# Kernel optimization log

Hardware: AMD Instinct MI355X
Metric: run time of the kernel (lower is better)

Reference implementation:

```python
import jax, jax.numpy as jnp
import numpy as np

B, N, D, E, HEADS = 2, 256, 768, 8192, 8
HD = D // HEADS
EPS = 1e-5


def _lin(x, w, b):
    return x @ w.T + b


def setup_inputs() -> dict:
    key = jax.random.key(0)
    ks = iter(jax.random.split(key, 64))

    def W(*s):
        return jax.random.normal(next(ks), s, jnp.float32) * 0.02

    inp = {
        "node_embeddings": jax.random.normal(next(ks), (B, N, D), jnp.float32),
        "edge_weights": jax.random.uniform(next(ks), (E,), jnp.float32),
        "edge_indices": jax.random.randint(next(ks), (E, 2), 0, N, jnp.int32),
        # object classifier: D->D->D//2->8
        "oc_w1": W(D, D), "oc_b1": jnp.zeros((D,), jnp.float32),
        "oc_w2": W(D // 2, D), "oc_b2": jnp.zeros((D // 2,), jnp.float32),
        "oc_w3": W(8, D // 2), "oc_b3": jnp.zeros((8,), jnp.float32),
        # importance predictor: D->D//2->D//4->1
        "ip_w1": W(D // 2, D), "ip_b1": jnp.zeros((D // 2,), jnp.float32),
        "ip_w2": W(D // 4, D // 2), "ip_b2": jnp.zeros((D // 4,), jnp.float32),
        "ip_w3": W(1, D // 4), "ip_b3": jnp.zeros((1,), jnp.float32),
        # relation classifier: 2D->D->D//2->8
        "rc_w1": W(D, 2 * D), "rc_b1": jnp.zeros((D,), jnp.float32),
        "rc_w2": W(D // 2, D), "rc_b2": jnp.zeros((D // 2,), jnp.float32),
        "rc_w3": W(8, D // 2), "rc_b3": jnp.zeros((8,), jnp.float32),
        # attention in/out projections
        "attn_in_w": W(3 * D, D), "attn_in_b": jnp.zeros((3 * D,), jnp.float32),
        "attn_out_w": W(D, D), "attn_out_b": jnp.zeros((D,), jnp.float32),
    }
    for l in range(3):
        inp[f"gnn{l}_ws"] = W(D, D)
        inp[f"gnn{l}_bs"] = jnp.zeros((D,), jnp.float32)
        inp[f"gnn{l}_wn"] = W(D, D)
        inp[f"gnn{l}_bn"] = jnp.zeros((D,), jnp.float32)
        inp[f"gnn{l}_g"] = jnp.ones((D,), jnp.float32)
        inp[f"gnn{l}_beta"] = jnp.zeros((D,), jnp.float32)
    return inp


def reference(node_embeddings, edge_weights, edge_indices,
              oc_w1, oc_b1, oc_w2, oc_b2, oc_w3, oc_b3,
              ip_w1, ip_b1, ip_w2, ip_b2, ip_w3, ip_b3,
              rc_w1, rc_b1, rc_w2, rc_b2, rc_w3, rc_b3,
              attn_in_w, attn_in_b, attn_out_w, attn_out_b,
              gnn0_ws, gnn0_bs, gnn0_wn, gnn0_bn, gnn0_g, gnn0_beta,
              gnn1_ws, gnn1_bs, gnn1_wn, gnn1_bn, gnn1_g, gnn1_beta,
              gnn2_ws, gnn2_bs, gnn2_wn, gnn2_bn, gnn2_g, gnn2_beta):
    x = node_embeddings  # [B,N,D]
    src, tgt = edge_indices[:, 0], edge_indices[:, 1]

    # object classifier (dropout is identity in eval)
    h = jax.nn.relu(_lin(x, oc_w1, oc_b1))
    h = jax.nn.relu(_lin(h, oc_w2, oc_b2))
    object_cls = jax.nn.softmax(_lin(h, oc_w3, oc_b3), axis=-1)

    # importance predictor
    h = jax.nn.relu(_lin(x, ip_w1, ip_b1))
    h = jax.nn.relu(_lin(h, ip_w2, ip_b2))
    importance = jax.nn.sigmoid(_lin(h, ip_w3, ip_b3))

    # 3 GNN layers: self-linear + weighted scatter-add neighbor aggregation
    g = x
    layers = [(gnn0_ws, gnn0_bs, gnn0_wn, gnn0_bn, gnn0_g, gnn0_beta),
              (gnn1_ws, gnn1_bs, gnn1_wn, gnn1_bn, gnn1_g, gnn1_beta),
              (gnn2_ws, gnn2_bs, gnn2_wn, gnn2_bn, gnn2_g, gnn2_beta)]
    for ws, bs, wn, bn, gm, bt in layers:
        self_f = _lin(g, ws, bs)
        # vectorized scatter-add: agg[b,tgt] += w_e * g[b,src]
        agg = jnp.zeros_like(g).at[:, tgt, :].add(edge_weights[None, :, None] * g[:, src, :])
        neigh_f = _lin(agg, wn, bn)
        o = jax.nn.relu(self_f + neigh_f)
        mu = o.mean(axis=-1, keepdims=True)
        var = o.var(axis=-1, keepdims=True)  # biased, as torch LayerNorm
        g = gm * (o - mu) / jnp.sqrt(var + EPS) + bt

    # multi-head self-attention (torch MultiheadAttention, batch_first)
    qkv = _lin(g, attn_in_w, attn_in_b)  # [B,N,3D]
    q, k, v = jnp.split(qkv, 3, axis=-1)

    def heads(t):
        return t.reshape(B, N, HEADS, HD).transpose(0, 2, 1, 3)  # [B,H,N,hd]

    q, k, v = heads(q), heads(k), heads(v)
    scores = jnp.einsum('bhqd,bhkd->bhqk', q, k) / jnp.sqrt(jnp.float32(HD))
    attn = jax.nn.softmax(scores, axis=-1)
    ctx = jnp.einsum('bhqk,bhkd->bhqd', attn, v).transpose(0, 2, 1, 3).reshape(B, N, D)
    attended = _lin(ctx, attn_out_w, attn_out_b)  # [B,N,D]
    attn_weights = attn.mean(axis=1)  # torch averages heads -> [B,N,N]

    # all O(N^2) upper-triangular pairs, same (i<j) row-major order as the loop
    ii, jj = np.triu_indices(N, k=1)
    pair = jnp.concatenate([attended[:, ii, :], attended[:, jj, :]], axis=-1)  # [B,P,2D]
    h = jax.nn.relu(_lin(pair, rc_w1, rc_b1))
    h = jax.nn.relu(_lin(h, rc_w2, rc_b2))
    relation = jax.nn.softmax(_lin(h, rc_w3, rc_b3), axis=-1)  # [B,P,8]

    return (object_cls, relation, importance, attended, attn_weights)
```

## Files before the change

kernel.cpp:

```cpp
#include <hip/hip_runtime.h>
#include <hip/hip_bf16.h>

typedef __bf16 bf16;
typedef __bf16 bf16x4 __attribute__((ext_vector_type(4)));
typedef __bf16 bf16x8 __attribute__((ext_vector_type(8)));
typedef float  f32x4  __attribute__((ext_vector_type(4)));

#define NB 2
#define NN 256
#define DD 768
#define EE 8192
#define NPAIR 32640

__device__ inline float wred_sum(float v) {
#pragma unroll
  for (int o = 32; o > 0; o >>= 1) v += __shfl_down(v, o, 64);
  return v;
}
__device__ inline float wred_max(float v) {
#pragma unroll
  for (int o = 32; o > 0; o >>= 1) v = fmaxf(v, __shfl_down(v, o, 64));
  return v;
}

typedef const __attribute__((address_space(1))) void GASV;
typedef __attribute__((address_space(3))) void LASV;
__device__ __forceinline__ void async_cp16(const void* g, void* l) {
  __builtin_amdgcn_global_load_lds((GASV*)g, (LASV*)l, 16, 0, 0);
}

struct CJob { const float* s; bf16* d; int n; };
struct CJobs { CJob j[15]; };
__global__ __launch_bounds__(256) void convert_jobs(CJobs jobs) {
  const CJob jb = jobs.j[blockIdx.y];
  int nv = jb.n >> 2;
  for (int i = blockIdx.x * 256 + threadIdx.x; i < nv; i += gridDim.x * 256) {
    float4 v = ((const float4*)jb.s)[i];
    bf16x4 pk = { (bf16)v.x, (bf16)v.y, (bf16)v.z, (bf16)v.w };
    *(bf16x4*)(jb.d + 4 * i) = pk;
  }
}

__device__ __forceinline__ void lin_body(
    const bf16* __restrict__ X, const bf16* __restrict__ W, int ldw, int wofs,
    const float* __restrict__ bias, const float* __restrict__ addF,
    bf16* __restrict__ outB, float* __restrict__ outF,
    int N, int K, int act)
{
  int tid = threadIdx.x;
  int wave = tid >> 6, lane = tid & 63, lr = lane & 15, lq = lane >> 4;
  int m0 = (blockIdx.x * 2 + wave) * 16;
  int n0 = blockIdx.y * 32;
  const bf16* xrow = X + (size_t)(m0 + lr) * K;
  const bf16* wbase = W + (size_t)wofs;
  f32x4 acc[2] = {};
  for (int k = 0; k < K; k += 32) {
    bf16x8 a = *(const bf16x8*)(xrow + k + lq * 8);
    bf16x8 b0 = *(const bf16x8*)(wbase + (size_t)(n0 + lr) * ldw + k + lq * 8);
    bf16x8 b1 = *(const bf16x8*)(wbase + (size_t)(n0 + 16 + lr) * ldw + k + lq * 8);
    acc[0] = __builtin_amdgcn_mfma_f32_16x16x32_bf16(a, b0, acc[0], 0, 0, 0);
    acc[1] = __builtin_amdgcn_mfma_f32_16x16x32_bf16(a, b1, acc[1], 0, 0, 0);
  }
#pragma unroll
  for (int t = 0; t < 2; ++t) {
    int col = n0 + t * 16 + lr;
    float bv = bias ? bias[col] : 0.0f;
#pragma unroll
    for (int r = 0; r < 4; ++r) {
      int row = m0 + lq * 4 + r;
      size_t o = (size_t)row * N + col;
      float v = acc[t][r] + bv;
      if (addF) v += addF[o];
      if (act) v = fmaxf(v, 0.0f);
      if (outB) outB[o] = (bf16)v;
      if (outF) outF[o] = v;
    }
  }
}

__global__ __launch_bounds__(128) void linear_mfma(
    const bf16* __restrict__ X, const bf16* __restrict__ W, int ldw, int wofs,
    const float* __restrict__ bias, const float* __restrict__ addF,
    bf16* __restrict__ outB, float* __restrict__ outF,
    int N, int K, int act)
{
  lin_body(X, W, ldw, wofs, bias, addF, outB, outF, N, K, act);
}

struct LinJob {
  const bf16* X; const bf16* W; int ldw; int wofs;
  const float* bias; const float* addF; bf16* outB; float* outF;
  int N, K, act, gy;
};
__global__ __launch_bounds__(128) void linear_mfma2(LinJob j0, LinJob j1)
{
  LinJob j = blockIdx.z ? j1 : j0;
  if ((int)blockIdx.y >= j.gy) return;
  lin_body(j.X, j.W, j.ldw, j.wofs, j.bias, j.addF, j.outB, j.outF, j.N, j.K, j.act);
}

__global__ __launch_bounds__(256) void build_buckets(
    const int* __restrict__ eidx, int* __restrict__ estart, int* __restrict__ bucket)
{
  __shared__ int tg[EE];
  __shared__ int cnt[256];
  __shared__ int sst[257];
  int t = threadIdx.x;
  cnt[t] = 0;
  for (int e = t; e < EE; e += 256) tg[e] = eidx[2 * e + 1];
  __syncthreads();
  for (int e = t; e < EE; e += 256) atomicAdd(&cnt[tg[e]], 1);
  __syncthreads();
  if (t == 0) { int s = 0; for (int i = 0; i < 256; ++i) { sst[i] = s; s += cnt[i]; } sst[256] = s; }
  __syncthreads();
  estart[t] = sst[t];
  if (t == 0) estart[256] = sst[256];
  cnt[t] = sst[t];
  __syncthreads();
  for (int e = t; e < EE; e += 256) {
    int p = atomicAdd(&cnt[tg[e]], 1);
    bucket[p] = e;
  }
}

__global__ __launch_bounds__(256) void gnn_agg(
    const bf16* __restrict__ g, const float* __restrict__ ew, const int* __restrict__ eidx,
    const int* __restrict__ estart, const int* __restrict__ bucket, bf16* __restrict__ agg)
{
  __shared__ int   ssrc[256];
  __shared__ float sw[256];
  int tgt = blockIdx.x, b = blockIdx.y, t = threadIdx.x;
  int s = estart[tgt], e = estart[tgt + 1];
  s = max(0, min(s, EE));
  e = max(s, min(e, EE));
  const bf16* gb = g + (size_t)b * NN * DD;
  float a0 = 0, a1 = 0, a2 = 0, a3 = 0;
  for (int base = s; base < e; base += 256) {
    int nchunk = min(256, e - base);
    if (t < nchunk) {
      int eid = bucket[base + t];
      eid = max(0, min(eid, EE - 1));
      ssrc[t] = eidx[2 * eid] & (NN - 1);
      sw[t] = ew[eid];
    }
    __syncthreads();
    if (t < 192) {
      for (int q = 0; q < nchunk; ++q) {
        float w = sw[q];
        bf16x4 v = *(const bf16x4*)(gb + (size_t)ssrc[q] * DD + 4 * t);
        a0 += w * (float)v[0]; a1 += w * (float)v[1];
        a2 += w * (float)v[2]; a3 += w * (float)v[3];
      }
    }
    __syncthreads();
  }
  if (t < 192) {
    bf16x4 o = { (bf16)a0, (bf16)a1, (bf16)a2, (bf16)a3 };
    *(bf16x4*)(agg + ((size_t)b * NN + tgt) * DD + 4 * t) = o;
  }
}

__global__ __launch_bounds__(256) void layer_norm(
    const float* __restrict__ o, const float* __restrict__ gm,
    const float* __restrict__ bt, bf16* __restrict__ gout)
{
  __shared__ float red[8];
  int row = blockIdx.x, t = threadIdx.x;
  const float* orow = o + (size_t)row * DD;
  float v0 = orow[t], v1 = orow[t + 256], v2 = orow[t + 512];
  float s = v0 + v1 + v2;
  float q = v0 * v0 + v1 * v1 + v2 * v2;
  float ws_ = wred_sum(s), wq = wred_sum(q);
  if ((t & 63) == 0) { red[t >> 6] = ws_; red[4 + (t >> 6)] = wq; }
  __syncthreads();
  float S = red[0] + red[1] + red[2] + red[3];
  float Q = red[4] + red[5] + red[6] + red[7];
  float mu = S * (1.0f / 768.0f);
  float var = Q * (1.0f / 768.0f) - mu * mu;
  float rstd = rsqrtf(var + 1e-5f);
  bf16* gr = gout + (size_t)row * DD;
  gr[t]       = (bf16)(gm[t]       * (v0 - mu) * rstd + bt[t]);
  gr[t + 256] = (bf16)(gm[t + 256] * (v1 - mu) * rstd + bt[t + 256]);
  gr[t + 512] = (bf16)(gm[t + 512] * (v2 - mu) * rstd + bt[t + 512]);
}

__global__ __launch_bounds__(256) void attn_kernel(
    const bf16* __restrict__ qkv, float* __restrict__ aw, bf16* __restrict__ ctx)
{
  __shared__ float qs[96];
  __shared__ float ps[256];
  __shared__ float part[192];
  __shared__ float red[8];
  int qi = blockIdx.x, h = blockIdx.y, b = blockIdx.z, t = threadIdx.x;
  const bf16* qrow = qkv + ((size_t)(b * NN + qi)) * 2304 + h * 96;
  if (t < 96) qs[t] = (float)qrow[t];
  __syncthreads();
  const bf16* krow = qkv + ((size_t)(b * NN + t)) * 2304 + 768 + h * 96;
  float s = 0;
#pragma unroll
  for (int i = 0; i < 12; ++i) {
    bf16x8 kv = *(const bf16x8*)(krow + 8 * i);
#pragma unroll
    for (int j = 0; j < 8; ++j) s += qs[8 * i + j] * (float)kv[j];
  }
  s *= 0.10206207261596577f;
  float wm = wred_max(s);
  if ((t & 63) == 0) red[t >> 6] = wm;
  __syncthreads();
  float MX = fmaxf(fmaxf(red[0], red[1]), fmaxf(red[2], red[3]));
  float e = expf(s - MX);
  float wsum = wred_sum(e);
  if ((t & 63) == 0) red[4 + (t >> 6)] = wsum;
  __syncthreads();
  float SUM = red[4] + red[5] + red[6] + red[7];
  float p = e / SUM;
  ps[t] = p;
  atomicAdd(&aw[((size_t)(b * NN + qi)) * NN + t], p * 0.125f);
  __syncthreads();
  if (t < 192) {
    int d = t % 96, half = t / 96;
    const bf16* vbase = qkv + (size_t)b * NN * 2304 + 1536 + h * 96 + d;
    float a0 = 0, a1 = 0, a2 = 0, a3 = 0;
    int k0 = half * 128;
    for (int k = k0; k < k0 + 128; k += 4) {
      a0 += ps[k]     * (float)vbase[(size_t)k * 2304];
      a1 += ps[k + 1] * (float)vbase[(size_t)(k + 1) * 2304];
      a2 += ps[k + 2] * (float)vbase[(size_t)(k + 2) * 2304];
      a3 += ps[k + 3] * (float)vbase[(size_t)(k + 3) * 2304];
    }
    part[t] = (a0 + a1) + (a2 + a3);
  }
  __syncthreads();
  if (t < 96)
    ctx[((size_t)(b * NN + qi)) * DD + h * 96 + t] = (bf16)(part[t] + part[t + 96]);
}

__global__ __launch_bounds__(256) void fc8_softmax(
    const bf16* __restrict__ h, const float* __restrict__ w,
    const float* __restrict__ bias, float* __restrict__ out)
{
  __shared__ float sw3[8 * 384];
  int t = threadIdx.x;
  for (int i = t; i < 8 * 384; i += 256) sw3[i] = w[i];
  __syncthreads();
  int wave = t >> 6, lane = t & 63;
  int k0 = lane * 6;
#pragma unroll
  for (int i = 0; i < 4; ++i) {
    int r = blockIdx.x * 16 + wave * 4 + i;
    const bf16* hr = h + (size_t)r * 384;
    float hv[6];
#pragma unroll
    for (int j = 0; j < 6; ++j) hv[j] = (float)hr[k0 + j];
    float lg[8];
#pragma unroll
    for (int c = 0; c < 8; ++c) {
      float p = 0;
#pragma unroll
      for (int j = 0; j < 6; ++j) p += hv[j] * sw3[c * 384 + k0 + j];
      lg[c] = wred_sum(p);
    }
    if (lane == 0) {
      float mx = lg[0] + bias[0];
#pragma unroll
      for (int c = 0; c < 8; ++c) { lg[c] += bias[c]; mx = fmaxf(mx, lg[c]); }
      float ex[8], sum = 0;
#pragma unroll
      for (int c = 0; c < 8; ++c) { ex[c] = expf(lg[c] - mx); sum += ex[c]; }
      float inv = 1.0f / sum;
#pragma unroll
      for (int c = 0; c < 8; ++c) out[(size_t)r * 8 + c] = ex[c] * inv;
    }
  }
}

__global__ __launch_bounds__(256) void fc1_sigmoid(
    const bf16* __restrict__ h, const float* __restrict__ w,
    const float* __restrict__ bias, float* __restrict__ out)
{
  __shared__ float sw1[192];
  int t = threadIdx.x;
  if (t < 192) sw1[t] = w[t];
  __syncthreads();
  int wave = t >> 6, lane = t & 63;
  int k0 = lane * 3;
#pragma unroll
  for (int i = 0; i < 4; ++i) {
    int r = blockIdx.x * 16 + wave * 4 + i;
    const bf16* hr = h + (size_t)r * 192;
    float p = (float)hr[k0] * sw1[k0] + (float)hr[k0 + 1] * sw1[k0 + 1]
            + (float)hr[k0 + 2] * sw1[k0 + 2];
    float s = wred_sum(p);
    if (lane == 0) out[r] = 1.0f / (1.0f + expf(-(s + bias[0])));
  }
}

__global__ void make_pairs(int2* __restrict__ pairs)
{
  int i = blockIdx.x;
  int off = i * 255 - (i * (i - 1)) / 2;
  for (int j = i + 1 + threadIdx.x; j < NN; j += blockDim.x)
    pairs[off + (j - i - 1)] = make_int2(i, j);
}

__global__ __launch_bounds__(256) void h2_gemm(
    const bf16* __restrict__ Af, const bf16* __restrict__ Bf,
    const bf16* __restrict__ w2, const float* __restrict__ b2,
    const int2* __restrict__ pairs, bf16* __restrict__ h2)
{
  __shared__ bf16 sh1[4][128][8];
  __shared__ bf16 sw2[4][192][8];
  __shared__ int rA[128], rB[128];
  int tid = threadIdx.x;
  int r0 = blockIdx.x * 128;
  int bb = (r0 >= NPAIR) ? 1 : 0;
  int n0 = blockIdx.y * 192;
  if (tid < 128) {
    int2 ij = pairs[r0 - bb * NPAIR + tid];
    rA[tid] = (bb * NN + ij.x) * DD;
    rB[tid] = (bb * NN + ij.y) * DD;
  }
  __syncthreads();
  int hrow = tid >> 1, hp = (tid & 1) * 2;
  const bf16* ar = Af + rA[hrow] + hp * 8;
  const bf16* br = Bf + rB[hrow] + hp * 8;
  int pl[3], rw[3];
#pragma unroll
  for (int q = 0; q < 3; ++q) {
    int a = q * 256 + tid;
    pl[q] = a / 192;
    rw[q] = a - pl[q] * 192;
  }
  int wave = tid >> 6, lane = tid & 63, lr = lane & 15, lq = lane >> 4;
  int wr = wave >> 1, wc = wave & 1;
  f32x4 acc[4][6] = {};
  for (int k0 = 0; k0 < 768; k0 += 32) {
#pragma unroll
    for (int q = 0; q < 3; ++q)
      async_cp16(w2 + (size_t)(n0 + rw[q]) * 768 + k0 + pl[q] * 8,
                 (char*)sw2 + (q * 256 + tid) * 16);
    bf16x8 a0 = *(const bf16x8*)(ar + k0);
    bf16x8 a1 = *(const bf16x8*)(ar + k0 + 8);
    bf16x8 b0 = *(const bf16x8*)(br + k0);
    bf16x8 b1 = *(const bf16x8*)(br + k0 + 8);
    bf16x8 h0, h1v;
#pragma unroll
    for (int j = 0; j < 8; ++j) {
      h0[j]  = (bf16)fmaxf((float)a0[j] + (float)b0[j], 0.f);
      h1v[j] = (bf16)fmaxf((float)a1[j] + (float)b1[j], 0.f);
    }
    *(bf16x8*)&sh1[hp][hrow][0] = h0;
    *(bf16x8*)&sh1[hp + 1][hrow][0] = h1v;
    __syncthreads();
    bf16x8 af[4], bfr[6];
#pragma unroll
    for (int rf = 0; rf < 4; ++rf)
      af[rf] = *(const bf16x8*)&sh1[lq][wr * 64 + rf * 16 + lr][0];
#pragma unroll
    for (int cf = 0; cf < 6; ++cf)
      bfr[cf] = *(const bf16x8*)&sw2[lq][wc * 96 + cf * 16 + lr][0];
#pragma unroll
    for (int rf = 0; rf < 4; ++rf)
#pragma unroll
      for (int cf = 0; cf < 6; ++cf)
        acc[rf][cf] = __builtin_amdgcn_mfma_f32_16x16x32_bf16(af[rf], bfr[cf], acc[rf][cf], 0, 0, 0);
    __syncthreads();
  }
#pragma unroll
  for (int cf = 0; cf < 6; ++cf) {
    int col = n0 + wc * 96 + cf * 16 + lr;
    float bv2 = b2[col];
#pragma unroll
    for (int rf = 0; rf < 4; ++rf)
#pragma unroll
      for (int r = 0; r < 4; ++r) {
        int prow = r0 + wr * 64 + rf * 16 + lq * 4 + r;
        h2[(size_t)prow * 384 + col] = (bf16)fmaxf(acc[rf][cf][r] + bv2, 0.f);
      }
  }
}

extern "C" void kernel_launch(void* const* d_in, const int* in_sizes, int n_in,
                              void* d_out, int out_size, void* d_ws, size_t ws_size,
                              hipStream_t stream)
{
  (void)in_sizes; (void)n_in; (void)out_size; (void)ws_size;
  const float* x    = (const float*)d_in[0];
  const float* ew   = (const float*)d_in[1];
  const int*   eidx = (const int*)d_in[2];
  const float* oc_w1 = (const float*)d_in[3];  const float* oc_b1 = (const float*)d_in[4];
  const float* oc_w2 = (const float*)d_in[5];  const float* oc_b2 = (const float*)d_in[6];
  const float* oc_w3 = (const float*)d_in[7];  const float* oc_b3 = (const float*)d_in[8];
  const float* ip_w1 = (const float*)d_in[9];  const float* ip_b1 = (const float*)d_in[10];
  const float* ip_w2 = (const float*)d_in[11]; const float* ip_b2 = (const float*)d_in[12];
  const float* ip_w3 = (const float*)d_in[13]; const float* ip_b3 = (const float*)d_in[14];
  const float* rc_w1 = (const float*)d_in[15]; const float* rc_b1 = (const float*)d_in[16];
  const float* rc_w2 = (const float*)d_in[17]; const float* rc_b2 = (const float*)d_in[18];
  const float* rc_w3 = (const float*)d_in[19]; const float* rc_b3 = (const float*)d_in[20];
  const float* at_iw = (const float*)d_in[21]; const float* at_ib = (const float*)d_in[22];
  const float* at_ow = (const float*)d_in[23]; const float* at_ob = (const float*)d_in[24];

  float* out = (float*)d_out;
  float* out_oc  = out;
  float* out_rel = out + 4096;
  float* out_imp = out + 526336;
  float* out_att = out + 526848;
  float* out_aw  = out + 920064;

  char* wp = (char*)d_ws;
  auto alloc = [&](size_t bytes) { char* p = wp; wp += (bytes + 255) & ~(size_t)255; return p; };
  bf16* h2B  = (bf16*)alloc((size_t)(2 * NPAIR) * 384 * 2);
  float* selfF = (float*)alloc((size_t)512 * 768 * 4);
  float* oBuf  = (float*)alloc((size_t)512 * 768 * 4);
  bf16* AfB  = (bf16*)alloc((size_t)512 * 768 * 2);
  bf16* BfB  = (bf16*)alloc((size_t)512 * 768 * 2);
  bf16* xb   = (bf16*)alloc((size_t)512 * 768 * 2);
  bf16* g0   = (bf16*)alloc((size_t)512 * 768 * 2);
  bf16* g1   = (bf16*)alloc((size_t)512 * 768 * 2);
  bf16* hA   = (bf16*)alloc((size_t)512 * 768 * 2);
  bf16* hB   = (bf16*)alloc((size_t)512 * 384 * 2);
  bf16* hI1  = (bf16*)alloc((size_t)512 * 384 * 2);
  bf16* hI2  = (bf16*)alloc((size_t)512 * 192 * 2);
  bf16* aggB = (bf16*)alloc((size_t)512 * 768 * 2);
  bf16* qkv  = (bf16*)alloc((size_t)512 * 2304 * 2);
  bf16* ctx  = (bf16*)alloc((size_t)512 * 768 * 2);
  bf16* attB = (bf16*)alloc((size_t)512 * 768 * 2);
  bf16* w_oc1 = (bf16*)alloc((size_t)768 * 768 * 2);
  bf16* w_oc2 = (bf16*)alloc((size_t)384 * 768 * 2);
  bf16* w_ip1 = (bf16*)alloc((size_t)384 * 768 * 2);
  bf16* w_ip2 = (bf16*)alloc((size_t)192 * 384 * 2);
  bf16* w_rc1 = (bf16*)alloc((size_t)768 * 1536 * 2);
  bf16* w_rc2 = (bf16*)alloc((size_t)384 * 768 * 2);
  bf16* w_aiw = (bf16*)alloc((size_t)2304 * 768 * 2);
  bf16* w_aow = (bf16*)alloc((size_t)768 * 768 * 2);
  bf16* w_gnn[6];
  for (int i = 0; i < 6; ++i) w_gnn[i] = (bf16*)alloc((size_t)768 * 768 * 2);
  int2* pairs = (int2*)alloc((size_t)NPAIR * 8);
  int* estart = (int*)alloc(257 * 4);
  int* bucket = (int*)alloc((size_t)EE * 4);

  dim3 blk(256);
  dim3 blk128(128);

  CJobs cj;
  cj.j[0]  = { x,     xb,    512 * 768 };
  cj.j[1]  = { oc_w1, w_oc1, 768 * 768 };
  cj.j[2]  = { oc_w2, w_oc2, 384 * 768 };
  cj.j[3]  = { ip_w1, w_ip1, 384 * 768 };
  cj.j[4]  = { ip_w2, w_ip2, 192 * 384 };
  cj.j[5]  = { rc_w1, w_rc1, 768 * 1536 };
  cj.j[6]  = { rc_w2, w_rc2, 384 * 768 };
  cj.j[7]  = { at_iw, w_aiw, 2304 * 768 };
  cj.j[8]  = { at_ow, w_aow, 768 * 768 };
  for (int l = 0; l < 3; ++l) {
    cj.j[9 + 2 * l]  = { (const float*)d_in[25 + l * 6 + 0], w_gnn[2 * l],     768 * 768 };
    cj.j[10 + 2 * l] = { (const float*)d_in[25 + l * 6 + 2], w_gnn[2 * l + 1], 768 * 768 };
  }
  convert_jobs<<<dim3(128, 15), blk, 0, stream>>>(cj);
  hipMemsetAsync(out_aw, 0, (size_t)NB * NN * NN * 4, stream);

  build_buckets<<<1, blk, 0, stream>>>(eidx, estart, bucket);
  make_pairs<<<255, blk, 0, stream>>>(pairs);

  {
    LinJob a = { xb, w_oc1, 768, 0, oc_b1, nullptr, hA,  nullptr, 768, 768, 1, 24 };
    LinJob b = { xb, w_ip1, 768, 0, ip_b1, nullptr, hI1, nullptr, 384, 768, 1, 12 };
    linear_mfma2<<<dim3(16, 24, 2), blk128, 0, stream>>>(a, b);
  }
  {
    LinJob a = { hA,  w_oc2, 768, 0, oc_b2, nullptr, hB,  nullptr, 384, 768, 1, 12 };
    LinJob b = { hI1, w_ip2, 384, 0, ip_b2, nullptr, hI2, nullptr, 192, 384, 1, 6 };
    linear_mfma2<<<dim3(16, 12, 2), blk128, 0, stream>>>(a, b);
  }
  fc8_softmax<<<32, blk, 0, stream>>>(hB, oc_w3, oc_b3, out_oc);
  fc1_sigmoid<<<32, blk, 0, stream>>>(hI2, ip_w3, ip_b3, out_imp);

  const bf16* gcur = xb;
  bf16* gbufs[2] = { g0, g1 };
  for (int l = 0; l < 3; ++l) {
    const float* bs_ = (const float*)d_in[25 + l * 6 + 1];
    const float* bn_ = (const float*)d_in[25 + l * 6 + 3];
    const float* gm_ = (const float*)d_in[25 + l * 6 + 4];
    const float* bt_ = (const float*)d_in[25 + l * 6 + 5];
    linear_mfma<<<dim3(16, 24), blk128, 0, stream>>>(gcur, w_gnn[2 * l], 768, 0, bs_, nullptr, nullptr, selfF, 768, 768, 0);
    gnn_agg<<<dim3(256, 2), blk, 0, stream>>>(gcur, ew, eidx, estart, bucket, aggB);
    linear_mfma<<<dim3(16, 24), blk128, 0, stream>>>(aggB, w_gnn[2 * l + 1], 768, 0, bn_, selfF, nullptr, oBuf, 768, 768, 1);
    layer_norm<<<512, blk, 0, stream>>>(oBuf, gm_, bt_, gbufs[l & 1]);
    gcur = gbufs[l & 1];
  }

  linear_mfma<<<dim3(16, 72), blk128, 0, stream>>>(gcur, w_aiw, 768, 0, at_ib, nullptr, qkv, nullptr, 2304, 768, 0);
  attn_kernel<<<dim3(256, 8, 2), blk, 0, stream>>>(qkv, out_aw, ctx);
  linear_mfma<<<dim3(16, 24), blk128, 0, stream>>>(ctx, w_aow, 768, 0, at_ob, nullptr, attB, out_att, 768, 768, 0);

  {
    LinJob a = { attB, w_rc1, 1536, 0,   rc_b1,  nullptr, AfB, nullptr, 768, 768, 0, 24 };
    LinJob b = { attB, w_rc1, 1536, 768, nullptr, nullptr, BfB, nullptr, 768, 768, 0, 24 };
    linear_mfma2<<<dim3(16, 24, 2), blk128, 0, stream>>>(a, b);
  }
  h2_gemm<<<dim3(510, 2), blk, 0, stream>>>(AfB, BfB, w_rc2, rc_b2, pairs, h2B);
  fc8_softmax<<<4080, blk, 0, stream>>>(h2B, rc_w3, rc_b3, out_rel);
}
```

Baseline: 539.4 us.

## Merge independent launches into combined kernels and remap h2_gemm LDS layout

```diff
diff --git a/kernel.cpp b/kernel.cpp
--- a/kernel.cpp
+++ b/kernel.cpp
@@ -31,26 +31,58 @@
 
 struct CJob { const float* s; bf16* d; int n; };
 struct CJobs { CJob j[15]; };
-__global__ __launch_bounds__(256) void convert_jobs(CJobs jobs) {
-  const CJob jb = jobs.j[blockIdx.y];
-  int nv = jb.n >> 2;
-  for (int i = blockIdx.x * 256 + threadIdx.x; i < nv; i += gridDim.x * 256) {
-    float4 v = ((const float4*)jb.s)[i];
-    bf16x4 pk = { (bf16)v.x, (bf16)v.y, (bf16)v.z, (bf16)v.w };
-    *(bf16x4*)(jb.d + 4 * i) = pk;
-  }
-}
-
-__device__ __forceinline__ void lin_body(
-    const bf16* __restrict__ X, const bf16* __restrict__ W, int ldw, int wofs,
-    const float* __restrict__ bias, const float* __restrict__ addF,
-    bf16* __restrict__ outB, float* __restrict__ outF,
-    int N, int K, int act)
-{
-  int tid = threadIdx.x;
-  int wave = tid >> 6, lane = tid & 63, lr = lane & 15, lq = lane >> 4;
-  int m0 = (blockIdx.x * 2 + wave) * 16;
-  int n0 = blockIdx.y * 32;
+__global__ __launch_bounds__(256) void preamble(
+    CJobs jobs, const int* __restrict__ eidx, int* __restrict__ estart,
+    int* __restrict__ bucket, int2* __restrict__ pairs)
+{
+  int by = blockIdx.y, t = threadIdx.x;
+  if (by < 15) {
+    const CJob jb = jobs.j[by];
+    int nv = jb.n >> 2;
+    for (int i = blockIdx.x * 256 + t; i < nv; i += gridDim.x * 256) {
+      float4 v = ((const float4*)jb.s)[i];
+      bf16x4 pk = { (bf16)v.x, (bf16)v.y, (bf16)v.z, (bf16)v.w };
+      *(bf16x4*)(jb.d + 4 * i) = pk;
+    }
+  } else if (by == 15) {
+    if (blockIdx.x != 0) return;
+    __shared__ int tg[EE];
+    __shared__ int cnt[256];
+    __shared__ int sst[257];
+    cnt[t] = 0;
+    for (int e = t; e < EE; e += 256) tg[e] = eidx[2 * e + 1];
+    __syncthreads();
+    for (int e = t; e < EE; e += 256) atomicAdd(&cnt[tg[e]], 1);
+    __syncthreads();
+    if (t == 0) { int s = 0; for (int i = 0; i < 256; ++i) { sst[i] = s; s += cnt[i]; } sst[256] = s; }
+    __syncthreads();
+    estart[t] = sst[t];
+    if (t == 0) estart[256] = sst[256];
+    cnt[t] = sst[t];
+    __syncthreads();
+    for (int e = t; e < EE; e += 256) {
+      int p = atomicAdd(&cnt[tg[e]], 1);
+      bucket[p] = e;
+    }
+  } else {
+#pragma unroll
+    for (int u = 0; u < 2; ++u) {
+      int i = blockIdx.x + u * 128;
+      if (i < 255) {
+        int off = i * 255 - (i * (i - 1)) / 2;
+        for (int j = i + 1 + t; j < NN; j += 256)
+          pairs[off + (j - i - 1)] = make_int2(i, j);
+      }
+    }
+  }
+}
+
+__device__ __forceinline__ void lin_core(
+    int m0, int n0, const bf16* __restrict__ X, const bf16* __restrict__ W,
+    int ldw, int wofs, const float* __restrict__ bias, const float* __restrict__ addF,
+    bf16* __restrict__ outB, float* __restrict__ outF, int N, int K, int act)
+{
+  int lane = threadIdx.x & 63, lr = lane & 15, lq = lane >> 4;
   const bf16* xrow = X + (size_t)(m0 + lr) * K;
   const bf16* wbase = W + (size_t)wofs;
   f32x4 acc[2] = {};
@@ -84,7 +116,9 @@
     bf16* __restrict__ outB, float* __restrict__ outF,
     int N, int K, int act)
 {
-  lin_body(X, W, ldw, wofs, bias, addF, outB, outF, N, K, act);
+  int wave = threadIdx.x >> 6;
+  lin_core((blockIdx.x * 2 + wave) * 16, blockIdx.y * 32,
+           X, W, ldw, wofs, bias, addF, outB, outF, N, K, act);
 }
 
 struct LinJob {
@@ -96,40 +130,28 @@
 {
   LinJob j = blockIdx.z ? j1 : j0;
   if ((int)blockIdx.y >= j.gy) return;
-  lin_body(j.X, j.W, j.ldw, j.wofs, j.bias, j.addF, j.outB, j.outF, j.N, j.K, j.act);
-}
-
-__global__ __launch_bounds__(256) void build_buckets(
-    const int* __restrict__ eidx, int* __restrict__ estart, int* __restrict__ bucket)
-{
-  __shared__ int tg[EE];
-  __shared__ int cnt[256];
-  __shared__ int sst[257];
-  int t = threadIdx.x;
-  cnt[t] = 0;
-  for (int e = t; e < EE; e += 256) tg[e] = eidx[2 * e + 1];
-  __syncthreads();
-  for (int e = t; e < EE; e += 256) atomicAdd(&cnt[tg[e]], 1);
-  __syncthreads();
-  if (t == 0) { int s = 0; for (int i = 0; i < 256; ++i) { sst[i] = s; s += cnt[i]; } sst[256] = s; }
-  __syncthreads();
-  estart[t] = sst[t];
-  if (t == 0) estart[256] = sst[256];
-  cnt[t] = sst[t];
-  __syncthreads();
-  for (int e = t; e < EE; e += 256) {
-    int p = atomicAdd(&cnt[tg[e]], 1);
-    bucket[p] = e;
-  }
-}
-
-__global__ __launch_bounds__(256) void gnn_agg(
-    const bf16* __restrict__ g, const float* __restrict__ ew, const int* __restrict__ eidx,
+  int wave = threadIdx.x >> 6;
+  lin_core((blockIdx.x * 2 + wave) * 16, blockIdx.y * 32,
+           j.X, j.W, j.ldw, j.wofs, j.bias, j.addF, j.outB, j.outF, j.N, j.K, j.act);
+}
+
+__global__ __launch_bounds__(256) void gnn_stage1(
+    const bf16* __restrict__ g, const bf16* __restrict__ ws, const float* __restrict__ bs,
+    float* __restrict__ selfF,
+    const float* __restrict__ ew, const int* __restrict__ eidx,
     const int* __restrict__ estart, const int* __restrict__ bucket, bf16* __restrict__ agg)
 {
+  int bid = blockIdx.x, t = threadIdx.x;
+  if (bid < 192) {
+    int wave = t >> 6;
+    lin_core(((bid & 7) * 4 + wave) * 16, (bid >> 3) * 32,
+             g, ws, 768, 0, bs, nullptr, nullptr, selfF, 768, 768, 0);
+    return;
+  }
   __shared__ int   ssrc[256];
   __shared__ float sw[256];
-  int tgt = blockIdx.x, b = blockIdx.y, t = threadIdx.x;
+  int e0 = bid - 192;
+  int tgt = e0 & 255, b = e0 >> 8;
   int s = estart[tgt], e = estart[tgt + 1];
   s = max(0, min(s, EE));
   e = max(s, min(e, EE));
@@ -274,33 +296,61 @@
   }
 }
 
-__global__ __launch_bounds__(256) void fc1_sigmoid(
-    const bf16* __restrict__ h, const float* __restrict__ w,
-    const float* __restrict__ bias, float* __restrict__ out)
-{
-  __shared__ float sw1[192];
+__global__ __launch_bounds__(256) void small_heads(
+    const bf16* __restrict__ hOC, const float* __restrict__ w3, const float* __restrict__ b3,
+    float* __restrict__ outOC,
+    const bf16* __restrict__ hIP, const float* __restrict__ w1, const float* __restrict__ b1,
+    float* __restrict__ outIP)
+{
   int t = threadIdx.x;
-  if (t < 192) sw1[t] = w[t];
-  __syncthreads();
   int wave = t >> 6, lane = t & 63;
-  int k0 = lane * 3;
-#pragma unroll
-  for (int i = 0; i < 4; ++i) {
-    int r = blockIdx.x * 16 + wave * 4 + i;
-    const bf16* hr = h + (size_t)r * 192;
-    float p = (float)hr[k0] * sw1[k0] + (float)hr[k0 + 1] * sw1[k0 + 1]
-            + (float)hr[k0 + 2] * sw1[k0 + 2];
-    float s = wred_sum(p);
-    if (lane == 0) out[r] = 1.0f / (1.0f + expf(-(s + bias[0])));
-  }
-}
-
-__global__ void make_pairs(int2* __restrict__ pairs)
-{
-  int i = blockIdx.x;
-  int off = i * 255 - (i * (i - 1)) / 2;
-  for (int j = i + 1 + threadIdx.x; j < NN; j += blockDim.x)
-    pairs[off + (j - i - 1)] = make_int2(i, j);
+  if (blockIdx.x < 32) {
+    __shared__ float sw3[8 * 384];
+    for (int i = t; i < 8 * 384; i += 256) sw3[i] = w3[i];
+    __syncthreads();
+    int k0 = lane * 6;
+#pragma unroll
+    for (int i = 0; i < 4; ++i) {
+      int r = blockIdx.x * 16 + wave * 4 + i;
+      const bf16* hr = hOC + (size_t)r * 384;
+      float hv[6];
+#pragma unroll
+      for (int j = 0; j < 6; ++j) hv[j] = (float)hr[k0 + j];
+      float lg[8];
+#pragma unroll
+      for (int c = 0; c < 8; ++c) {
+        float p = 0;
+#pragma unroll
+        for (int j = 0; j < 6; ++j) p += hv[j] * sw3[c * 384 + k0 + j];
+        lg[c] = wred_sum(p);
+      }
+      if (lane == 0) {
+        float mx = lg[0] + b3[0];
+#pragma unroll
+        for (int c = 0; c < 8; ++c) { lg[c] += b3[c]; mx = fmaxf(mx, lg[c]); }
+        float ex[8], sum = 0;
+#pragma unroll
+        for (int c = 0; c < 8; ++c) { ex[c] = expf(lg[c] - mx); sum += ex[c]; }
+        float inv = 1.0f / sum;
+#pragma unroll
+        for (int c = 0; c < 8; ++c) outOC[(size_t)r * 8 + c] = ex[c] * inv;
+      }
+    }
+  } else {
+    __shared__ float sw1[192];
+    if (t < 192) sw1[t] = w1[t];
+    __syncthreads();
+    int k0 = lane * 3;
+#pragma unroll
+    for (int i = 0; i < 4; ++i) {
+      int r = (blockIdx.x - 32) * 16 + wave * 4 + i;
+      const bf16* hr = hIP + (size_t)r * 192;
+      float p = (float)hr[k0] * sw1[k0] + (float)hr[k0 + 1] * sw1[k0 + 1]
+              + (float)hr[k0 + 2] * sw1[k0 + 2];
+      float s = wred_sum(p);
+      if (lane == 0) outIP[r] = 1.0f / (1.0f + expf(-(s + b1[0])));
+    }
+  }
 }
 
 __global__ __launch_bounds__(256) void h2_gemm(
@@ -308,8 +358,8 @@
     const bf16* __restrict__ w2, const float* __restrict__ b2,
     const int2* __restrict__ pairs, bf16* __restrict__ h2)
 {
-  __shared__ bf16 sh1[4][128][8];
-  __shared__ bf16 sw2[4][192][8];
+  __shared__ bf16x8 sh1[512];
+  __shared__ bf16x8 sw2[768];
   __shared__ int rA[128], rB[128];
   int tid = threadIdx.x;
   int r0 = blockIdx.x * 128;
@@ -324,12 +374,13 @@
   int hrow = tid >> 1, hp = (tid & 1) * 2;
   const bf16* ar = Af + rA[hrow] + hp * 8;
   const bf16* br = Bf + rB[hrow] + hp * 8;
-  int pl[3], rw[3];
+  int hslot = ((hrow >> 4) << 6) + (hp << 4) + (hrow & 15);
+  int srow[3], spl[3];
 #pragma unroll
   for (int q = 0; q < 3; ++q) {
     int a = q * 256 + tid;
-    pl[q] = a / 192;
-    rw[q] = a - pl[q] * 192;
+    srow[q] = ((a >> 6) << 4) + (a & 15);
+    spl[q] = (a >> 4) & 3;
   }
   int wave = tid >> 6, lane = tid & 63, lr = lane & 15, lq = lane >> 4;
   int wr = wave >> 1, wc = wave & 1;
@@ -337,7 +388,7 @@
   for (int k0 = 0; k0 < 768; k0 += 32) {
 #pragma unroll
     for (int q = 0; q < 3; ++q)
-      async_cp16(w2 + (size_t)(n0 + rw[q]) * 768 + k0 + pl[q] * 8,
+      async_cp16(w2 + (size_t)(n0 + srow[q]) * 768 + k0 + spl[q] * 8,
                  (char*)sw2 + (q * 256 + tid) * 16);
     bf16x8 a0 = *(const bf16x8*)(ar + k0);
     bf16x8 a1 = *(const bf16x8*)(ar + k0 + 8);
@@ -349,16 +400,16 @@
       h0[j]  = (bf16)fmaxf((float)a0[j] + (float)b0[j], 0.f);
       h1v[j] = (bf16)fmaxf((float)a1[j] + (float)b1[j], 0.f);
     }
-    *(bf16x8*)&sh1[hp][hrow][0] = h0;
-    *(bf16x8*)&sh1[hp + 1][hrow][0] = h1v;
+    sh1[hslot] = h0;
+    sh1[hslot + 16] = h1v;
     __syncthreads();
     bf16x8 af[4], bfr[6];
 #pragma unroll
     for (int rf = 0; rf < 4; ++rf)
-      af[rf] = *(const bf16x8*)&sh1[lq][wr * 64 + rf * 16 + lr][0];
+      af[rf] = sh1[(wr * 4 + rf) * 64 + lq * 16 + lr];
 #pragma unroll
     for (int cf = 0; cf < 6; ++cf)
-      bfr[cf] = *(const bf16x8*)&sw2[lq][wc * 96 + cf * 16 + lr][0];
+      bfr[cf] = sw2[(wc * 6 + cf) * 64 + lq * 16 + lr];
 #pragma unroll
     for (int rf = 0; rf < 4; ++rf)
 #pragma unroll
@@ -456,11 +507,8 @@
     cj.j[9 + 2 * l]  = { (const float*)d_in[25 + l * 6 + 0], w_gnn[2 * l],     768 * 768 };
     cj.j[10 + 2 * l] = { (const float*)d_in[25 + l * 6 + 2], w_gnn[2 * l + 1], 768 * 768 };
   }
-  convert_jobs<<<dim3(128, 15), blk, 0, stream>>>(cj);
   hipMemsetAsync(out_aw, 0, (size_t)NB * NN * NN * 4, stream);
-
-  build_buckets<<<1, blk, 0, stream>>>(eidx, estart, bucket);
-  make_pairs<<<255, blk, 0, stream>>>(pairs);
+  preamble<<<dim3(128, 17), blk, 0, stream>>>(cj, eidx, estart, bucket, pairs);
 
   {
     LinJob a = { xb, w_oc1, 768, 0, oc_b1, nullptr, hA,  nullptr, 768, 768, 1, 24 };
@@ -472,8 +520,7 @@
     LinJob b = { hI1, w_ip2, 384, 0, ip_b2, nullptr, hI2, nullptr, 192, 384, 1, 6 };
     linear_mfma2<<<dim3(16, 12, 2), blk128, 0, stream>>>(a, b);
   }
-  fc8_softmax<<<32, blk, 0, stream>>>(hB, oc_w3, oc_b3, out_oc);
-  fc1_sigmoid<<<32, blk, 0, stream>>>(hI2, ip_w3, ip_b3, out_imp);
+  small_heads<<<64, blk, 0, stream>>>(hB, oc_w3, oc_b3, out_oc, hI2, ip_w3, ip_b3, out_imp);
 
   const bf16* gcur = xb;
   bf16* gbufs[2] = { g0, g1 };
@@ -482,8 +529,7 @@
     const float* bn_ = (const float*)d_in[25 + l * 6 + 3];
     const float* gm_ = (const float*)d_in[25 + l * 6 + 4];
     const float* bt_ = (const float*)d_in[25 + l * 6 + 5];
-    linear_mfma<<<dim3(16, 24), blk128, 0, stream>>>(gcur, w_gnn[2 * l], 768, 0, bs_, nullptr, nullptr, selfF, 768, 768, 0);
-    gnn_agg<<<dim3(256, 2), blk, 0, stream>>>(gcur, ew, eidx, estart, bucket, aggB);
+    gnn_stage1<<<704, blk, 0, stream>>>(gcur, w_gnn[2 * l], bs_, selfF, ew, eidx, estart, bucket, aggB);
     linear_mfma<<<dim3(16, 24), blk128, 0, stream>>>(aggB, w_gnn[2 * l + 1], 768, 0, bn_, selfF, nullptr, oBuf, 768, 768, 1);
     layer_norm<<<512, blk, 0, stream>>>(oBuf, gm_, bt_, gbufs[l & 1]);
     gcur = gbufs[l & 1];
```

Result: faster. 511.0 us (-5.3%).
